# Performance work log

Measured on AMD Instinct MI355X. Metric: run time of the kernel, lower is better.

Reference implementation:

```python
import jax, jax.numpy as jnp
import numpy as np

N_NODES = 100000
N_EDGES = 1600000


def spmm(rows, cols, vals, z):
    # out[i] = sum_{e: rows[e]==i} vals[e] * z[cols[e]]  (COO sparse-dense matmul)
    msgs = vals[:, None] * z[cols]  # [E, d] gather + scale
    return jax.ops.segment_sum(msgs, rows, num_segments=N_NODES)


def setup_inputs() -> dict:
    key = jax.random.key(0)
    k1, k2, k3, k4, k5, k6, k7, k8 = jax.random.split(key, 8)
    rows = jax.random.randint(k1, (N_EDGES,), 0, N_NODES, dtype=jnp.int32)
    cols = jax.random.randint(k2, (N_EDGES,), 0, N_NODES, dtype=jnp.int32)
    vals = jax.random.uniform(k3, (N_EDGES,), dtype=jnp.float32)
    x = jax.random.normal(k4, (N_NODES, 128), dtype=jnp.float32)
    # Linear layers per n_feats = [128, 128, 64]; stored as [in, out] (z @ W + b)
    W1 = jax.random.normal(k5, (128, 128), dtype=jnp.float32) * (1.0 / np.sqrt(128))
    b1 = jax.random.normal(k6, (128,), dtype=jnp.float32) * 0.01
    W2 = jax.random.normal(k7, (128, 64), dtype=jnp.float32) * (1.0 / np.sqrt(128))
    b2 = jax.random.normal(k8, (64,), dtype=jnp.float32) * 0.01
    return {"rows": rows, "cols": cols, "vals": vals, "x": x,
            "W1": W1, "b1": b1, "W2": W2, "b2": b2}


def reference(rows, cols, vals, x, W1, b1, W2, b2):
    # layer 1: activation(spmm(a, linear(x)))
    z = jax.nn.relu(spmm(rows, cols, vals, x @ W1 + b1))
    # last layer: spmm(a, linear(z)) with no activation
    z = spmm(rows, cols, vals, z @ W2 + b2)
    return z
```

## Files before the change

kernel.cpp:

```cpp
#include <hip/hip_runtime.h>

typedef unsigned int uint;
typedef unsigned short ushort;
typedef unsigned long long u64;
typedef float f32x4 __attribute__((ext_vector_type(4)));
typedef short bf16x8 __attribute__((ext_vector_type(8)));

#define NN 100000
#define NE 1600000
#define NBUCK ((NN + 255) >> 8)
#define VSCALE (1.0f / 32768.0f)

__device__ __forceinline__ ushort f2bf(float f) {
    uint u = __float_as_uint(f);
    u += 0x7FFFu + ((u >> 16) & 1u);
    return (ushort)(u >> 16);
}
__device__ __forceinline__ float bf2f(ushort h) {
    return __uint_as_float(((uint)h) << 16);
}

__global__ __launch_bounds__(256) void prep_w_kernel(
    const float* __restrict__ W1, const float* __restrict__ W2,
    ushort* __restrict__ Wt1, ushort* __restrict__ Wt2)
{
    int t = blockIdx.x * 256 + threadIdx.x;
    if (t < 128 * 128) {
        int c = t & 127, k = t >> 7;
        Wt1[c * 128 + k] = f2bf(W1[k * 128 + c]);
    }
    if (t < 64 * 128) {
        int c = t & 63, k = t >> 6;
        Wt2[c * 128 + k] = f2bf(W2[k * 64 + c]);
    }
}

template <typename TIN, int M>
__global__ __launch_bounds__(256) void gemm_mfma(
    const TIN* __restrict__ X, const ushort* __restrict__ Wt,
    const float* __restrict__ b, ushort* __restrict__ Y, int N)
{
    constexpr int NT = M / 16;
    constexpr int PITCH = 136;
    __shared__ ushort xt[64 * PITCH];
    __shared__ ushort wt[M * PITCH];

    const int tid  = threadIdx.x;
    const int row0 = blockIdx.x * 64;

    for (int i = tid; i < M * 32; i += 256) {
        int c = i >> 5, kc = i & 31;
        u64 w4 = reinterpret_cast<const u64*>(Wt)[c * 32 + kc];
        *reinterpret_cast<u64*>(&wt[c * PITCH + kc * 4]) = w4;
    }
    for (int i = tid; i < 64 * 32; i += 256) {
        int r = i >> 5, kc = i & 31;
        int rr = row0 + r;
        if (rr >= N) rr = N - 1;
        ushort4 o;
        if constexpr (sizeof(TIN) == 4) {
            f32x4 v = __builtin_nontemporal_load(
                reinterpret_cast<const f32x4*>(X) + (size_t)rr * 32 + kc);
            o.x = f2bf(v.x); o.y = f2bf(v.y); o.z = f2bf(v.z); o.w = f2bf(v.w);
        } else {
            u64 v = reinterpret_cast<const u64*>(X)[(size_t)rr * 32 + kc];
            o.x = (ushort)v; o.y = (ushort)(v >> 16);
            o.z = (ushort)(v >> 32); o.w = (ushort)(v >> 48);
        }
        *reinterpret_cast<u64*>(&xt[r * PITCH + kc * 4]) =
            (u64)o.x | ((u64)o.y << 16) | ((u64)o.z << 32) | ((u64)o.w << 48);
    }
    __syncthreads();

    const int wave = tid >> 6, lane = tid & 63;
    const int lrow = lane & 15;
    const int kgrp = lane >> 4;

    bf16x8 a[4];
    #pragma unroll
    for (int ks = 0; ks < 4; ++ks)
        a[ks] = *reinterpret_cast<bf16x8*>(
            &xt[(wave * 16 + lrow) * PITCH + ks * 32 + kgrp * 8]);

    f32x4 acc[NT];
    #pragma unroll
    for (int nt = 0; nt < NT; ++nt) {
        float bv = b[nt * 16 + lrow];
        acc[nt].x = bv; acc[nt].y = bv; acc[nt].z = bv; acc[nt].w = bv;
    }

    #pragma unroll
    for (int nt = 0; nt < NT; ++nt) {
        #pragma unroll
        for (int ks = 0; ks < 4; ++ks) {
            bf16x8 bf = *reinterpret_cast<bf16x8*>(
                &wt[(nt * 16 + lrow) * PITCH + ks * 32 + kgrp * 8]);
            acc[nt] = __builtin_amdgcn_mfma_f32_16x16x32_bf16(a[ks], bf, acc[nt], 0, 0, 0);
        }
    }

    __syncthreads();
    #pragma unroll
    for (int nt = 0; nt < NT; ++nt) {
        #pragma unroll
        for (int j = 0; j < 4; ++j) {
            int rloc = wave * 16 + kgrp * 4 + j;
            xt[rloc * PITCH + nt * 16 + lrow] = f2bf(acc[nt][j]);
        }
    }
    __syncthreads();
    for (int i = tid; i < 64 * (M / 4); i += 256) {
        int r  = i / (M / 4);
        int c4 = i % (M / 4);
        int rr = row0 + r;
        if (rr < N) {
            u64 o = *reinterpret_cast<u64*>(&xt[r * PITCH + c4 * 4]);
            *reinterpret_cast<u64*>(&Y[(size_t)rr * M + c4 * 4]) = o;
        }
    }
}

__global__ __launch_bounds__(256) void bucket_hist_kernel(
    const int* __restrict__ rows, int* __restrict__ gcnt)
{
    __shared__ int cnt[4][NBUCK];
    const int tid = threadIdx.x;
    const int sub = tid & 3;
    for (int i = tid; i < 4 * NBUCK; i += 256) cnt[i / NBUCK][i % NBUCK] = 0;
    __syncthreads();
    #pragma unroll
    for (int q = 0; q < 4; ++q) {
        int vi = blockIdx.x * 1024 + q * 256 + tid;
        if (vi < NE / 4) {
            int4 r = reinterpret_cast<const int4*>(rows)[vi];
            atomicAdd(&cnt[sub][r.x >> 8], 1); atomicAdd(&cnt[sub][r.y >> 8], 1);
            atomicAdd(&cnt[sub][r.z >> 8], 1); atomicAdd(&cnt[sub][r.w >> 8], 1);
        }
    }
    __syncthreads();
    for (int i = tid; i < NBUCK; i += 256) {
        int s = cnt[0][i] + cnt[1][i] + cnt[2][i] + cnt[3][i];
        if (s) atomicAdd(&gcnt[i], s);
    }
}

__global__ __launch_bounds__(512) void scan_kernel(
    const int* __restrict__ gcnt, int* __restrict__ bstart, int* __restrict__ gfill)
{
    __shared__ int s[512];
    const int tid = threadIdx.x;
    int v = (tid < NBUCK) ? gcnt[tid] : 0;
    s[tid] = v;
    __syncthreads();
    for (int off = 1; off < 512; off <<= 1) {
        int t = (tid >= off) ? s[tid - off] : 0;
        __syncthreads();
        s[tid] += t;
        __syncthreads();
    }
    if (tid < NBUCK) {
        bstart[tid] = s[tid] - v;
        gfill[tid]  = s[tid] - v;
    }
    if (tid == 0) bstart[NBUCK] = NE;
}

__global__ __launch_bounds__(1024) void bin_kernel(
    const int* __restrict__ rows, const int* __restrict__ cols,
    const float* __restrict__ vals, int* __restrict__ gfill,
    u64* __restrict__ es_stage)
{
    __shared__ int cnt[NBUCK];
    __shared__ int base[NBUCK];
    const int tid = threadIdx.x;

    for (int i = tid; i < NBUCK; i += 1024) cnt[i] = 0;
    __syncthreads();

    int r[8];
    #pragma unroll
    for (int q = 0; q < 8; ++q) {
        int e = blockIdx.x * 8192 + q * 1024 + tid;
        r[q] = (e < NE) ? rows[e] : -1;
        if (r[q] >= 0) atomicAdd(&cnt[r[q] >> 8], 1);
    }
    __syncthreads();

    for (int i = tid; i < NBUCK; i += 1024)
        base[i] = cnt[i] ? atomicAdd(&gfill[i], cnt[i]) : 0;
    __syncthreads();
    for (int i = tid; i < NBUCK; i += 1024) cnt[i] = 0;
    __syncthreads();

    #pragma unroll
    for (int q = 0; q < 8; ++q) {
        if (r[q] >= 0) {
            int e = blockIdx.x * 8192 + q * 1024 + tid;
            int bk = r[q] >> 8;
            int pos = base[bk] + atomicAdd(&cnt[bk], 1);
            uint lo = (uint)(r[q] & 255) | ((uint)cols[e] << 8);
            es_stage[pos] = (u64)lo | ((u64)(uint)__float_as_uint(vals[e]) << 32);
        }
    }
}

__global__ __launch_bounds__(1024) void finalize_kernel(
    const int* __restrict__ bstart, const u64* __restrict__ es_stage,
    int* __restrict__ row_ptr, uint* __restrict__ es)
{
    __shared__ int cnt[256];
    __shared__ int scn[256];
    __shared__ int fill[256];
    const int b    = blockIdx.x;
    const int tid  = threadIdx.x;
    const int row0 = b << 8;
    const int s = bstart[b];
    const int e = bstart[b + 1];

    if (tid < 256) cnt[tid] = 0;
    __syncthreads();

    for (int i = s + tid; i < e; i += 1024)
        atomicAdd(&cnt[(uint)es_stage[i] & 255u], 1);
    __syncthreads();

    if (tid < 256) scn[tid] = cnt[tid];
    __syncthreads();
    for (int off = 1; off < 256; off <<= 1) {
        int t = (tid < 256 && tid >= off) ? scn[tid - off] : 0;
        __syncthreads();
        if (tid < 256) scn[tid] += t;
        __syncthreads();
    }
    if (tid < 256) {
        int start = s + scn[tid] - cnt[tid];
        fill[tid] = start;
        int rr = row0 + tid;
        if (rr <= NN) row_ptr[rr] = start;
    }
    __syncthreads();

    for (int i = s + tid; i < e; i += 1024) {
        u64 pk = es_stage[i];
        uint lo = (uint)pk;
        int pos = atomicAdd(&fill[lo & 255u], 1);
        float v = __uint_as_float((uint)(pk >> 32));
        uint q = (uint)(v * 32768.f + 0.5f);
        if (q > 32767u) q = 32767u;
        es[pos] = ((lo >> 8) << 15) | q;
    }
}

template <int D, bool BF16_RELU_OUT>
__global__ __launch_bounds__(256) void spmm_gather(
    const int* __restrict__ row_ptr, const uint* __restrict__ es,
    const ushort* __restrict__ Zb, void* __restrict__ outv)
{
    const int row  = (blockIdx.x * 256 + threadIdx.x) >> 6;
    const int lane = threadIdx.x & 63;
    if (row >= NN) return;
    const int start = row_ptr[row];
    const int end   = row_ptr[row + 1];

    float accx = 0.f, accy = 0.f;

    for (int base = start; base < end; base += 64) {
        const int m = min(end - base, 64);
        int pk_l = (lane < m) ? (int)es[base + lane] : 0;

        int j = 0;
        for (; j + 8 <= m; j += 8) {
            uint pk[8];
            #pragma unroll
            for (int q = 0; q < 8; ++q) pk[q] = (uint)__shfl(pk_l, j + q);
            if (D == 128) {
                uint z[8];
                #pragma unroll
                for (int q = 0; q < 8; ++q)
                    z[q] = *reinterpret_cast<const uint*>(
                        &Zb[(size_t)(pk[q] >> 15) * 128 + 2 * lane]);
                #pragma unroll
                for (int q = 0; q < 8; ++q) {
                    float vf = (float)(pk[q] & 0x7FFFu);
                    accx += vf * __uint_as_float(z[q] << 16);
                    accy += vf * __uint_as_float(z[q] & 0xFFFF0000u);
                }
            } else {
                float z[8];
                #pragma unroll
                for (int q = 0; q < 8; ++q)
                    z[q] = bf2f(Zb[(size_t)(pk[q] >> 15) * 64 + lane]);
                #pragma unroll
                for (int q = 0; q < 8; ++q)
                    accx += (float)(pk[q] & 0x7FFFu) * z[q];
            }
        }
        for (; j < m; ++j) {
            uint pk = (uint)__shfl(pk_l, j);
            float vf = (float)(pk & 0x7FFFu);
            if (D == 128) {
                uint z = *reinterpret_cast<const uint*>(
                    &Zb[(size_t)(pk >> 15) * 128 + 2 * lane]);
                accx += vf * __uint_as_float(z << 16);
                accy += vf * __uint_as_float(z & 0xFFFF0000u);
            } else {
                accx += vf * bf2f(Zb[(size_t)(pk >> 15) * 64 + lane]);
            }
        }
    }

    accx *= VSCALE; accy *= VSCALE;

    if (BF16_RELU_OUT) {
        uint o = (uint)f2bf(fmaxf(accx, 0.f)) | ((uint)f2bf(fmaxf(accy, 0.f)) << 16);
        reinterpret_cast<uint*>(outv)[(size_t)row * 64 + lane] = o;
    } else if (D == 128) {
        float2 o = make_float2(accx, accy);
        *reinterpret_cast<float2*>(&reinterpret_cast<float*>(outv)[(size_t)row * 128 + 2 * lane]) = o;
    } else {
        __builtin_nontemporal_store(accx, &reinterpret_cast<float*>(outv)[(size_t)row * 64 + lane]);
    }
}

extern "C" void kernel_launch(void* const* d_in, const int* in_sizes, int n_in,
                              void* d_out, int out_size, void* d_ws, size_t ws_size,
                              hipStream_t stream)
{
    const int*   rows = (const int*)  d_in[0];
    const int*   cols = (const int*)  d_in[1];
    const float* vals = (const float*)d_in[2];
    const float* x    = (const float*)d_in[3];
    const float* W1   = (const float*)d_in[4];
    const float* b1   = (const float*)d_in[5];
    const float* W2   = (const float*)d_in[6];
    const float* b2   = (const float*)d_in[7];
    float* out = (float*)d_out;

    char* ws = (char*)d_ws;
    size_t off = 0;
    ushort* h1b    = (ushort*)(ws + off); off += (size_t)NN * 128 * sizeof(ushort);
    ushort* s1b    = (ushort*)(ws + off); off += (size_t)NN * 128 * sizeof(ushort);
    ushort* h2b    = (ushort*)(ws + off); off += (size_t)NN * 64 * sizeof(ushort);
    uint*   es     = (uint*)  (ws + off); off += (size_t)NE * sizeof(uint);
    int*    row_ptr= (int*)   (ws + off); off += (size_t)(NN + 1) * sizeof(int);
    int*    gcnt   = (int*)   (ws + off); off += (size_t)NBUCK * sizeof(int);
    int*    bstart = (int*)   (ws + off); off += (size_t)(NBUCK + 1) * sizeof(int);
    int*    gfill  = (int*)   (ws + off); off += (size_t)NBUCK * sizeof(int);
    ushort* Wt1    = (ushort*)(ws + off); off += (size_t)128 * 128 * sizeof(ushort);
    ushort* Wt2    = (ushort*)(ws + off); off += (size_t)64 * 128 * sizeof(ushort);
    u64*    es_stage = (u64*)h1b;

    hipMemsetAsync(gcnt, 0, (size_t)NBUCK * sizeof(int), stream);
    prep_w_kernel<<<64, 256, 0, stream>>>(W1, W2, Wt1, Wt2);
    bucket_hist_kernel<<<(NE / 4 + 1023) / 1024, 256, 0, stream>>>(rows, gcnt);
    scan_kernel<<<1, 512, 0, stream>>>(gcnt, bstart, gfill);
    bin_kernel<<<(NE + 8191) / 8192, 1024, 0, stream>>>(rows, cols, vals, gfill, es_stage);
    finalize_kernel<<<NBUCK, 1024, 0, stream>>>(bstart, es_stage, row_ptr, es);

    gemm_mfma<float, 128><<<(NN + 63) / 64, 256, 0, stream>>>(x, Wt1, b1, h1b, NN);
    spmm_gather<128, true><<<(NN * 64 + 255) / 256, 256, 0, stream>>>(row_ptr, es, h1b, s1b);

    gemm_mfma<ushort, 64><<<(NN + 63) / 64, 256, 0, stream>>>(s1b, Wt2, b2, h2b, NN);
    spmm_gather<64, false><<<(NN * 64 + 255) / 256, 256, 0, stream>>>(row_ptr, es, h2b, out);
}
```

Measured before the change: 314.4 us.

## Fuse weight prep into histogram, vectorize binning, widen GEMM tiles

Folds the weight transpose/convert kernel into the bucket histogram kernel, removing one launch. The bin kernel now has each thread load 8 contiguous rows/cols/vals with int4 loads instead of strided scalar loads. The finalize kernel unrolls its passes four-wide for more memory-level parallelism. The GEMM processes 128 rows per block (two 16-row MFMA tiles per wave), reusing the B fragments at the cost of more LDS per block and fewer blocks.

```diff
diff --git a/kernel.cpp b/kernel.cpp
--- a/kernel.cpp
+++ b/kernel.cpp
@@ -20,21 +20,6 @@
     return __uint_as_float(((uint)h) << 16);
 }
 
-__global__ __launch_bounds__(256) void prep_w_kernel(
-    const float* __restrict__ W1, const float* __restrict__ W2,
-    ushort* __restrict__ Wt1, ushort* __restrict__ Wt2)
-{
-    int t = blockIdx.x * 256 + threadIdx.x;
-    if (t < 128 * 128) {
-        int c = t & 127, k = t >> 7;
-        Wt1[c * 128 + k] = f2bf(W1[k * 128 + c]);
-    }
-    if (t < 64 * 128) {
-        int c = t & 63, k = t >> 6;
-        Wt2[c * 128 + k] = f2bf(W2[k * 64 + c]);
-    }
-}
-
 template <typename TIN, int M>
 __global__ __launch_bounds__(256) void gemm_mfma(
     const TIN* __restrict__ X, const ushort* __restrict__ Wt,
@@ -42,18 +27,18 @@
 {
     constexpr int NT = M / 16;
     constexpr int PITCH = 136;
-    __shared__ ushort xt[64 * PITCH];
+    __shared__ ushort xt[128 * PITCH];
     __shared__ ushort wt[M * PITCH];
 
     const int tid  = threadIdx.x;
-    const int row0 = blockIdx.x * 64;
+    const int row0 = blockIdx.x * 128;
 
     for (int i = tid; i < M * 32; i += 256) {
         int c = i >> 5, kc = i & 31;
         u64 w4 = reinterpret_cast<const u64*>(Wt)[c * 32 + kc];
         *reinterpret_cast<u64*>(&wt[c * PITCH + kc * 4]) = w4;
     }
-    for (int i = tid; i < 64 * 32; i += 256) {
+    for (int i = tid; i < 128 * 32; i += 256) {
         int r = i >> 5, kc = i & 31;
         int rr = row0 + r;
         if (rr >= N) rr = N - 1;
@@ -76,17 +61,23 @@
     const int lrow = lane & 15;
     const int kgrp = lane >> 4;
 
-    bf16x8 a[4];
-    #pragma unroll
-    for (int ks = 0; ks < 4; ++ks)
-        a[ks] = *reinterpret_cast<bf16x8*>(
-            &xt[(wave * 16 + lrow) * PITCH + ks * 32 + kgrp * 8]);
-
-    f32x4 acc[NT];
+    bf16x8 a[2][4];
+    #pragma unroll
+    for (int t = 0; t < 2; ++t)
+        #pragma unroll
+        for (int ks = 0; ks < 4; ++ks)
+            a[t][ks] = *reinterpret_cast<bf16x8*>(
+                &xt[(wave * 32 + t * 16 + lrow) * PITCH + ks * 32 + kgrp * 8]);
+
+    f32x4 acc[2][NT];
     #pragma unroll
     for (int nt = 0; nt < NT; ++nt) {
         float bv = b[nt * 16 + lrow];
-        acc[nt].x = bv; acc[nt].y = bv; acc[nt].z = bv; acc[nt].w = bv;
+        #pragma unroll
+        for (int t = 0; t < 2; ++t) {
+            acc[t][nt].x = bv; acc[t][nt].y = bv;
+            acc[t][nt].z = bv; acc[t][nt].w = bv;
+        }
     }
 
     #pragma unroll
@@ -95,21 +86,23 @@
         for (int ks = 0; ks < 4; ++ks) {
             bf16x8 bf = *reinterpret_cast<bf16x8*>(
                 &wt[(nt * 16 + lrow) * PITCH + ks * 32 + kgrp * 8]);
-            acc[nt] = __builtin_amdgcn_mfma_f32_16x16x32_bf16(a[ks], bf, acc[nt], 0, 0, 0);
-        }
-    }
-
-    __syncthreads();
-    #pragma unroll
-    for (int nt = 0; nt < NT; ++nt) {
+            acc[0][nt] = __builtin_amdgcn_mfma_f32_16x16x32_bf16(a[0][ks], bf, acc[0][nt], 0, 0, 0);
+            acc[1][nt] = __builtin_amdgcn_mfma_f32_16x16x32_bf16(a[1][ks], bf, acc[1][nt], 0, 0, 0);
+        }
+    }
+
+    __syncthreads();
+    #pragma unroll
+    for (int t = 0; t < 2; ++t)
         #pragma unroll
-        for (int j = 0; j < 4; ++j) {
-            int rloc = wave * 16 + kgrp * 4 + j;
-            xt[rloc * PITCH + nt * 16 + lrow] = f2bf(acc[nt][j]);
-        }
-    }
-    __syncthreads();
-    for (int i = tid; i < 64 * (M / 4); i += 256) {
+        for (int nt = 0; nt < NT; ++nt)
+            #pragma unroll
+            for (int j = 0; j < 4; ++j) {
+                int rloc = wave * 32 + t * 16 + kgrp * 4 + j;
+                xt[rloc * PITCH + nt * 16 + lrow] = f2bf(acc[t][nt][j]);
+            }
+    __syncthreads();
+    for (int i = tid; i < 128 * (M / 4); i += 256) {
         int r  = i / (M / 4);
         int c4 = i % (M / 4);
         int rr = row0 + r;
@@ -121,8 +114,22 @@
 }
 
 __global__ __launch_bounds__(256) void bucket_hist_kernel(
-    const int* __restrict__ rows, int* __restrict__ gcnt)
-{
+    const int* __restrict__ rows, int* __restrict__ gcnt,
+    const float* __restrict__ W1, const float* __restrict__ W2,
+    ushort* __restrict__ Wt1, ushort* __restrict__ Wt2)
+{
+    {
+        int t = blockIdx.x * 256 + threadIdx.x;
+        if (t < 128 * 128) {
+            int c = t & 127, k = t >> 7;
+            Wt1[c * 128 + k] = f2bf(W1[k * 128 + c]);
+        }
+        if (t < 64 * 128) {
+            int c = t & 63, k = t >> 6;
+            Wt2[c * 128 + k] = f2bf(W2[k * 64 + c]);
+        }
+    }
+
     __shared__ int cnt[4][NBUCK];
     const int tid = threadIdx.x;
     const int sub = tid & 3;
@@ -173,16 +180,30 @@
     __shared__ int cnt[NBUCK];
     __shared__ int base[NBUCK];
     const int tid = threadIdx.x;
+    const int e0  = blockIdx.x * 8192 + tid * 8;
 
     for (int i = tid; i < NBUCK; i += 1024) cnt[i] = 0;
     __syncthreads();
 
-    int r[8];
-    #pragma unroll
-    for (int q = 0; q < 8; ++q) {
-        int e = blockIdx.x * 8192 + q * 1024 + tid;
-        r[q] = (e < NE) ? rows[e] : -1;
-        if (r[q] >= 0) atomicAdd(&cnt[r[q] >> 8], 1);
+    int r[8], c[8]; float v[8];
+    int nval = 0;
+    if (e0 < NE) {
+        nval = min(NE - e0, 8);
+        int4 ra = reinterpret_cast<const int4*>(rows + e0)[0];
+        int4 rb = reinterpret_cast<const int4*>(rows + e0)[1];
+        int4 ca = reinterpret_cast<const int4*>(cols + e0)[0];
+        int4 cb = reinterpret_cast<const int4*>(cols + e0)[1];
+        f32x4 va = reinterpret_cast<const f32x4*>(vals + e0)[0];
+        f32x4 vb = reinterpret_cast<const f32x4*>(vals + e0)[1];
+        r[0]=ra.x; r[1]=ra.y; r[2]=ra.z; r[3]=ra.w;
+        r[4]=rb.x; r[5]=rb.y; r[6]=rb.z; r[7]=rb.w;
+        c[0]=ca.x; c[1]=ca.y; c[2]=ca.z; c[3]=ca.w;
+        c[4]=cb.x; c[5]=cb.y; c[6]=cb.z; c[7]=cb.w;
+        v[0]=va.x; v[1]=va.y; v[2]=va.z; v[3]=va.w;
+        v[4]=vb.x; v[5]=vb.y; v[6]=vb.z; v[7]=vb.w;
+        #pragma unroll
+        for (int q = 0; q < 8; ++q)
+            if (q < nval) atomicAdd(&cnt[r[q] >> 8], 1);
     }
     __syncthreads();
 
@@ -194,12 +215,11 @@
 
     #pragma unroll
     for (int q = 0; q < 8; ++q) {
-        if (r[q] >= 0) {
-            int e = blockIdx.x * 8192 + q * 1024 + tid;
+        if (q < nval) {
             int bk = r[q] >> 8;
             int pos = base[bk] + atomicAdd(&cnt[bk], 1);
-            uint lo = (uint)(r[q] & 255) | ((uint)cols[e] << 8);
-            es_stage[pos] = (u64)lo | ((u64)(uint)__float_as_uint(vals[e]) << 32);
+            uint lo = (uint)(r[q] & 255) | ((uint)c[q] << 8);
+            es_stage[pos] = (u64)lo | ((u64)(uint)__float_as_uint(v[q]) << 32);
         }
     }
 }
@@ -220,7 +240,18 @@
     if (tid < 256) cnt[tid] = 0;
     __syncthreads();
 
-    for (int i = s + tid; i < e; i += 1024)
+    int i = s + tid;
+    for (; i + 3072 < e; i += 4096) {
+        u64 p0 = es_stage[i];
+        u64 p1 = es_stage[i + 1024];
+        u64 p2 = es_stage[i + 2048];
+        u64 p3 = es_stage[i + 3072];
+        atomicAdd(&cnt[(uint)p0 & 255u], 1);
+        atomicAdd(&cnt[(uint)p1 & 255u], 1);
+        atomicAdd(&cnt[(uint)p2 & 255u], 1);
+        atomicAdd(&cnt[(uint)p3 & 255u], 1);
+    }
+    for (; i < e; i += 1024)
         atomicAdd(&cnt[(uint)es_stage[i] & 255u], 1);
     __syncthreads();
 
@@ -240,15 +271,29 @@
     }
     __syncthreads();
 
-    for (int i = s + tid; i < e; i += 1024) {
-        u64 pk = es_stage[i];
-        uint lo = (uint)pk;
-        int pos = atomicAdd(&fill[lo & 255u], 1);
-        float v = __uint_as_float((uint)(pk >> 32));
-        uint q = (uint)(v * 32768.f + 0.5f);
-        if (q > 32767u) q = 32767u;
-        es[pos] = ((lo >> 8) << 15) | q;
-    }
+#define EMIT(PK)                                                         \
+    {                                                                    \
+        uint lo = (uint)(PK);                                            \
+        int pos = atomicAdd(&fill[lo & 255u], 1);                        \
+        float vv = __uint_as_float((uint)((PK) >> 32));                  \
+        uint q = (uint)(vv * 32768.f + 0.5f);                            \
+        if (q > 32767u) q = 32767u;                                      \
+        es[pos] = ((lo >> 8) << 15) | q;                                 \
+    }
+
+    i = s + tid;
+    for (; i + 3072 < e; i += 4096) {
+        u64 p0 = es_stage[i];
+        u64 p1 = es_stage[i + 1024];
+        u64 p2 = es_stage[i + 2048];
+        u64 p3 = es_stage[i + 3072];
+        EMIT(p0) EMIT(p1) EMIT(p2) EMIT(p3)
+    }
+    for (; i < e; i += 1024) {
+        u64 p = es_stage[i];
+        EMIT(p)
+    }
+#undef EMIT
 }
 
 template <int D, bool BF16_RELU_OUT>
@@ -351,15 +396,15 @@
     u64*    es_stage = (u64*)h1b;
 
     hipMemsetAsync(gcnt, 0, (size_t)NBUCK * sizeof(int), stream);
-    prep_w_kernel<<<64, 256, 0, stream>>>(W1, W2, Wt1, Wt2);
-    bucket_hist_kernel<<<(NE / 4 + 1023) / 1024, 256, 0, stream>>>(rows, gcnt);
+    bucket_hist_kernel<<<(NE / 4 + 1023) / 1024, 256, 0, stream>>>(
+        rows, gcnt, W1, W2, Wt1, Wt2);
     scan_kernel<<<1, 512, 0, stream>>>(gcnt, bstart, gfill);
     bin_kernel<<<(NE + 8191) / 8192, 1024, 0, stream>>>(rows, cols, vals, gfill, es_stage);
     finalize_kernel<<<NBUCK, 1024, 0, stream>>>(bstart, es_stage, row_ptr, es);
 
-    gemm_mfma<float, 128><<<(NN + 63) / 64, 256, 0, stream>>>(x, Wt1, b1, h1b, NN);
+    gemm_mfma<float, 128><<<(NN + 127) / 128, 256, 0, stream>>>(x, Wt1, b1, h1b, NN);
     spmm_gather<128, true><<<(NN * 64 + 255) / 256, 256, 0, stream>>>(row_ptr, es, h1b, s1b);
 
-    gemm_mfma<ushort, 64><<<(NN + 63) / 64, 256, 0, stream>>>(s1b, Wt2, b2, h2b, NN);
+    gemm_mfma<ushort, 64><<<(NN + 127) / 128, 256, 0, stream>>>(s1b, Wt2, b2, h2b, NN);
     spmm_gather<64, false><<<(NN * 64 + 255) / 256, 256, 0, stream>>>(row_ptr, es, h2b, out);
 }
```

Result: no change. 309.5 us (-1.6%).
